# Optimization experiments

Measured on AMD Instinct MI355X. Metric: run time of the kernel, lower is better.

Reference implementation:

```python
import jax, jax.numpy as jnp
import numpy as np


def setup_inputs() -> dict:
    key = jax.random.key(0)
    ks = jax.random.split(key, 5)
    B, S, D = 4, 2048, 1024
    x = jax.random.normal(ks[0], (B, S, D), dtype=jnp.float32)
    wq = jax.random.normal(ks[1], (D, D), dtype=jnp.float32) * (D ** -0.5)
    wk = jax.random.normal(ks[2], (D, D), dtype=jnp.float32) * (D ** -0.5)
    wv = jax.random.normal(ks[3], (D, D), dtype=jnp.float32) * (D ** -0.5)
    wo = jax.random.normal(ks[4], (D, D), dtype=jnp.float32) * (D ** -0.5)
    return {"x": x, "wq": wq, "wk": wk, "wv": wv, "wo": wo, "n_heads": 16}


def reference(x, wq, wk, wv, wo, n_heads):
    B, S, D = x.shape
    hd = D // n_heads
    # projections (module computes x @ w.T)
    q = (x @ wq.T).reshape(B, S, n_heads, hd).transpose(0, 2, 1, 3)  # b h s d
    k = (x @ wk.T).reshape(B, S, n_heads, hd).transpose(0, 2, 1, 3)
    v = (x @ wv.T).reshape(B, S, n_heads, hd).transpose(0, 2, 1, 3)
    # NOTE: module scales by sqrt(d_model), not sqrt(head_dim)
    scores = jnp.einsum("bhqd,bhkd->bhqk", q, k) / jnp.sqrt(jnp.float32(D))
    # module bug preserved: masked_fill(mask == 0, -1e9) with mask = triu(diag=1)
    # fills positions where mask is False (lower triangle incl. diagonal).
    triu_mask = jnp.triu(jnp.ones((S, S), dtype=bool), k=1)  # True strictly above diag
    scores = jnp.where(triu_mask, scores, jnp.float32(-1e9))
    attn = jax.nn.softmax(scores, axis=-1)
    out = jnp.einsum("bhqk,bhkd->bhqd", attn, v)  # b h s d
    out = out.transpose(0, 2, 1, 3).reshape(B, S, D)
    return out @ wo.T
```

## Files before the change

kernel.cpp:

```cpp
#include <hip/hip_runtime.h>
#include <hip/hip_bf16.h>

typedef __attribute__((ext_vector_type(8))) short short8;
typedef __attribute__((ext_vector_type(4))) short bfx4;
typedef __attribute__((ext_vector_type(4))) float floatx4;
typedef __attribute__((ext_vector_type(4))) __fp16 h4_t;
typedef __attribute__((ext_vector_type(2))) __fp16 h2_t;
typedef __attribute__((ext_vector_type(8))) __fp16 h8_t;

#define BATCH 4
#define SEQ 2048
#define D_MODEL 1024
#define NH 16
#define HD 64
#define ELEMS 8388608
#define WELEMS 1048576

__device__ __forceinline__ unsigned short f2bf(float f) {
    union { float f; unsigned u; } x; x.f = f;
    unsigned r = x.u + 0x7FFFu + ((x.u >> 16) & 1u);
    return (unsigned short)(r >> 16);
}
__device__ __forceinline__ unsigned short f2h(float f) {
    union { __fp16 h; unsigned short u; } x;
    x.h = (__fp16)f;
    return x.u;
}

#if __has_builtin(__builtin_amdgcn_exp2f)
__device__ __forceinline__ float fexp2(float x) { return __builtin_amdgcn_exp2f(x); }
#else
__device__ __forceinline__ float fexp2(float x) { return exp2f(x); }
#endif

__device__ __forceinline__ void gll16(const void* g, const void* l) {
    __builtin_amdgcn_global_load_lds(
        (const __attribute__((address_space(1))) void*)g,
        (__attribute__((address_space(3))) void*)l,
        16, 0, 0);
}

__global__ __launch_bounds__(256)
void cvt_kernel(const float* __restrict__ x,  const float* __restrict__ wq,
                const float* __restrict__ wk, const float* __restrict__ wv,
                const float* __restrict__ wo,
                unsigned short* __restrict__ xbf,
                unsigned short* __restrict__ wqkv,
                unsigned short* __restrict__ wobf)
{
    size_t idx = ((size_t)blockIdx.x * 256 + threadIdx.x) * 8;
    const float* src; unsigned short* dst; size_t off;
    if (idx < (size_t)ELEMS)                    { src = x;  dst = xbf;             off = idx; }
    else if (idx < (size_t)ELEMS + WELEMS)      { src = wq; dst = wqkv;            off = idx - ELEMS; }
    else if (idx < (size_t)ELEMS + 2 * WELEMS)  { src = wk; dst = wqkv + WELEMS;   off = idx - ELEMS - WELEMS; }
    else if (idx < (size_t)ELEMS + 3 * WELEMS)  { src = wv; dst = wqkv + 2*WELEMS; off = idx - ELEMS - 2*WELEMS; }
    else                                        { src = wo; dst = wobf;            off = idx - ELEMS - 3*WELEMS; }
    floatx4 a = *(const floatx4*)(src + off);
    floatx4 b = *(const floatx4*)(src + off + 4);
    short8 v;
#pragma unroll
    for (int d = 0; d < 4; d++) { v[d] = (short)f2bf(a[d]); v[4+d] = (short)f2bf(b[d]); }
    *(short8*)(dst + off) = v;
}

__global__ __launch_bounds__(256, 2)
void gemm_qkv2_kernel(const unsigned short* __restrict__ A,
                      const unsigned short* __restrict__ B,
                      unsigned short* __restrict__ Qb,
                      unsigned short* __restrict__ Kb,
                      unsigned short* __restrict__ Vb)
{
    __shared__ __align__(16) unsigned short As[128 * 64];
    __shared__ __align__(16) unsigned short Bs[256 * 64];

    const int t = threadIdx.x;
    const int wave = t >> 6, lane = t & 63;
    const int lm = lane & 15, lq = lane >> 4;
    const int wrow = (wave >> 1) * 64, wcol = (wave & 1) * 128;
    const int m0 = blockIdx.x * 128, n0 = blockIdx.y * 256;
    const int lrow = lane >> 3, lg = lane & 7;
    const int gsw = lg ^ lrow;

    floatx4 acc[4][8] = {};

    for (int k0 = 0; k0 < 1024; k0 += 64) {
        __syncthreads();
#pragma unroll
        for (int i = 0; i < 4; i++) {
            int rows8 = wave * 32 + i * 8;
            gll16(A + (size_t)(m0 + rows8 + lrow) * 1024 + k0 + gsw * 8, As + rows8 * 64);
        }
#pragma unroll
        for (int i = 0; i < 8; i++) {
            int rows8 = wave * 64 + i * 8;
            gll16(B + (size_t)(n0 + rows8 + lrow) * 1024 + k0 + gsw * 8, Bs + rows8 * 64);
        }
        __syncthreads();

#pragma unroll
        for (int c = 0; c < 2; c++) {
            short8 af[4], bfr[8];
#pragma unroll
            for (int i = 0; i < 4; i++) {
                int ra = wrow + i * 16 + lm;
                int g = c * 4 + lq;
                af[i] = *(const short8*)(As + (ra * 8 + (g ^ (ra & 7))) * 8);
            }
#pragma unroll
            for (int j = 0; j < 8; j++) {
                int rb = wcol + j * 16 + lm;
                int g = c * 4 + lq;
                bfr[j] = *(const short8*)(Bs + (rb * 8 + (g ^ (rb & 7))) * 8);
            }
#pragma unroll
            for (int i = 0; i < 4; i++)
#pragma unroll
                for (int j = 0; j < 8; j++)
                    acc[i][j] = __builtin_amdgcn_mfma_f32_16x16x32_bf16(
                        af[i], bfr[j], acc[i][j], 0, 0, 0);
        }
    }

    const int z = n0 >> 10;
#pragma unroll
    for (int i = 0; i < 4; i++)
#pragma unroll
        for (int j = 0; j < 8; j++)
#pragma unroll
            for (int r = 0; r < 4; r++) {
                int gm = m0 + wrow + i * 16 + lq * 4 + r;
                int gn = n0 + wcol + j * 16 + lm;
                int nl = gn & 1023, h = nl >> 6, d = nl & 63;
                int b = gm >> 11, s = gm & 2047;
                float v = acc[i][j][r];
                size_t bh = (size_t)(b * NH + h);
                if (z == 0)      Qb[(bh * SEQ + s) * HD + d] = f2bf(v);
                else if (z == 1) Kb[(bh * SEQ + s) * HD + d] = f2bf(v);
                else             Vb[(bh * HD + d) * SEQ + s] = f2h(v);
            }
}

__global__ __launch_bounds__(256, 2)
void gemm_out2_kernel(const unsigned short* __restrict__ A,
                      const unsigned short* __restrict__ B,
                      float* __restrict__ Out)
{
    __shared__ __align__(16) unsigned short As[128 * 64];
    __shared__ __align__(16) unsigned short Bs[256 * 64];

    const int t = threadIdx.x;
    const int wave = t >> 6, lane = t & 63;
    const int lm = lane & 15, lq = lane >> 4;
    const int wrow = (wave >> 1) * 64, wcol = (wave & 1) * 128;
    const int m0 = blockIdx.x * 128, n0 = blockIdx.y * 256;
    const int lrow = lane >> 3, lg = lane & 7;
    const int gsw = lg ^ lrow;

    floatx4 acc[4][8] = {};

    for (int k0 = 0; k0 < 1024; k0 += 64) {
        __syncthreads();
#pragma unroll
        for (int i = 0; i < 4; i++) {
            int rows8 = wave * 32 + i * 8;
            gll16(A + (size_t)(m0 + rows8 + lrow) * 1024 + k0 + gsw * 8, As + rows8 * 64);
        }
#pragma unroll
        for (int i = 0; i < 8; i++) {
            int rows8 = wave * 64 + i * 8;
            gll16(B + (size_t)(n0 + rows8 + lrow) * 1024 + k0 + gsw * 8, Bs + rows8 * 64);
        }
        __syncthreads();

#pragma unroll
        for (int c = 0; c < 2; c++) {
            short8 af[4], bfr[8];
#pragma unroll
            for (int i = 0; i < 4; i++) {
                int ra = wrow + i * 16 + lm;
                int g = c * 4 + lq;
                af[i] = *(const short8*)(As + (ra * 8 + (g ^ (ra & 7))) * 8);
            }
#pragma unroll
            for (int j = 0; j < 8; j++) {
                int rb = wcol + j * 16 + lm;
                int g = c * 4 + lq;
                bfr[j] = *(const short8*)(Bs + (rb * 8 + (g ^ (rb & 7))) * 8);
            }
#pragma unroll
            for (int i = 0; i < 4; i++)
#pragma unroll
                for (int j = 0; j < 8; j++)
                    acc[i][j] = __builtin_amdgcn_mfma_f32_16x16x32_bf16(
                        af[i], bfr[j], acc[i][j], 0, 0, 0);
        }
    }

#pragma unroll
    for (int i = 0; i < 4; i++)
#pragma unroll
        for (int j = 0; j < 8; j++)
#pragma unroll
            for (int r = 0; r < 4; r++) {
                int gm = m0 + wrow + i * 16 + lq * 4 + r;
                int gn = n0 + wcol + j * 16 + lm;
                Out[(size_t)gm * D_MODEL + gn] = acc[i][j][r];
            }
}

#define PROCESS_Q(QI, BQ, ACC, LACC, DOMASK, KT)                               \
    do {                                                                       \
        _Pragma("unroll")                                                      \
        for (int jt = 0; jt < 8; jt++) {                                       \
            floatx4 sc = {};                                                   \
            _Pragma("unroll")                                                  \
            for (int c = 0; c < 2; c++) {                                      \
                int row_ = jt * 16 + lm;                                       \
                int g_ = c * 4 + lq;                                           \
                short8 kf = *(const short8*)(Ks + (row_ * 8 + (g_ ^ (row_ & 7))) * 8); \
                sc = __builtin_amdgcn_mfma_f32_16x16x32_bf16(kf, BQ[c], sc, 0, 0, 0); \
            }                                                                  \
            if (DOMASK) {                                                      \
                _Pragma("unroll")                                              \
                for (int r = 0; r < 4; r++) {                                  \
                    int kj = (KT) * 128 + jt * 16 + lq * 4 + r;                \
                    if (!(kj > (QI))) sc[r] = -3.2e10f;                        \
                }                                                              \
            }                                                                  \
            float p0 = fexp2(sc[0] * kA), p1 = fexp2(sc[1] * kA);              \
            float p2 = fexp2(sc[2] * kA), p3 = fexp2(sc[3] * kA);              \
            LACC += (p0 + p1) + (p2 + p3);                                     \
            h2_t a01 = __builtin_amdgcn_cvt_pkrtz(p0, p1);                     \
            h2_t a23 = __builtin_amdgcn_cvt_pkrtz(p2, p3);                     \
            h4_t pf;                                                           \
            pf[0] = a01[0]; pf[1] = a01[1]; pf[2] = a23[0]; pf[3] = a23[1];    \
            _Pragma("unroll")                                                  \
            for (int jd = 0; jd < 4; jd++) {                                   \
                int rowv_ = jd * 16 + lm;                                      \
                int g16_ = jt * 2 + (lq >> 1);                                 \
                int slot_ = rowv_ * 16 + (g16_ ^ lm);                          \
                h4_t vf = *(const h4_t*)((const __fp16*)Vs + slot_ * 8 + (lq & 1) * 4); \
                ACC[jd] = __builtin_amdgcn_mfma_f32_16x16x16f16(vf, pf, ACC[jd], 0, 0, 0); \
            }                                                                  \
        }                                                                      \
    } while (0)

__global__ __launch_bounds__(256, 2)
void attn5_kernel(const unsigned short* __restrict__ Q,
                  const unsigned short* __restrict__ K,
                  const unsigned short* __restrict__ V,
                  unsigned short* __restrict__ O)
{
    __shared__ __align__(16) unsigned short Ks[128 * 64];
    __shared__ __align__(16) unsigned short Vs[64 * 128];

    const int t = threadIdx.x;
    const int wave = t >> 6, lane = t & 63;
    const int lm = lane & 15, lq = lane >> 4;
    const int bh = blockIdx.y;
    const int jlo = blockIdx.x, jhi = 31 - jlo;
    const int qlo = jlo * 64 + wave * 16 + lm;
    const int qhi = jhi * 64 + wave * 16 + lm;

    const unsigned short* Qh = Q + (size_t)bh * SEQ * HD;
    const unsigned short* Kh = K + (size_t)bh * SEQ * HD;
    const unsigned short* Vh = V + (size_t)bh * HD * SEQ;

    short8 bq_lo[2], bq_hi[2];
    bq_lo[0] = *(const short8*)(Qh + (size_t)qlo * HD + lq * 8);
    bq_lo[1] = *(const short8*)(Qh + (size_t)qlo * HD + 32 + lq * 8);
    bq_hi[0] = *(const short8*)(Qh + (size_t)qhi * HD + lq * 8);
    bq_hi[1] = *(const short8*)(Qh + (size_t)qhi * HD + 32 + lq * 8);

    floatx4 acc_lo[4] = {}, acc_hi[4] = {};
    float l_lo = 0.f, l_hi = 0.f;
    const float kA = 0.04508422002778011f;

    const int lrow = lane >> 3, lg = lane & 7;
    const int kt_min = jlo >> 1;
    const int kthi_min = 15 - kt_min;

    for (int kt = 15; kt >= kt_min; kt--) {
        __syncthreads();
#pragma unroll
        for (int i = 0; i < 4; i++) {
            int rows8 = wave * 32 + i * 8;
            gll16(Kh + (size_t)(kt * 128 + rows8 + lrow) * HD + (lg ^ lrow) * 8,
                  Ks + rows8 * 64);
        }
#pragma unroll
        for (int i = 0; i < 4; i++) {
            int rows4 = wave * 16 + i * 4;
            int row = rows4 + (lane >> 4);
            int g = (lane & 15) ^ (row & 15);
            gll16(Vh + (size_t)row * SEQ + kt * 128 + g * 8, Vs + rows4 * 128);
        }
        __syncthreads();

        PROCESS_Q(qlo, bq_lo, acc_lo, l_lo, (kt == kt_min), kt);
        if (kt >= kthi_min)
            PROCESS_Q(qhi, bq_hi, acc_hi, l_hi, (kt == kthi_min), kt);
    }

    const int b = bh >> 4, h = bh & 15;
    {
        float l = l_lo;
        l += __shfl_xor(l, 16); l += __shfl_xor(l, 32);
        float inv = 1.0f / l;
#pragma unroll
        for (int jd = 0; jd < 4; jd++) {
            bfx4 o;
#pragma unroll
            for (int r = 0; r < 4; r++) o[r] = (short)f2bf(acc_lo[jd][r] * inv);
            *(bfx4*)(O + (size_t)(b * SEQ + qlo) * D_MODEL + h * HD + jd * 16 + lq * 4) = o;
        }
    }
    {
        float l = l_hi;
        l += __shfl_xor(l, 16); l += __shfl_xor(l, 32);
        float inv = 1.0f / l;
#pragma unroll
        for (int jd = 0; jd < 4; jd++) {
            bfx4 o;
#pragma unroll
            for (int r = 0; r < 4; r++) o[r] = (short)f2bf(acc_hi[jd][r] * inv);
            *(bfx4*)(O + (size_t)(b * SEQ + qhi) * D_MODEL + h * HD + jd * 16 + lq * 4) = o;
        }
    }
}

__global__ __launch_bounds__(256, 2)
void row2047_kernel(const unsigned short* __restrict__ V,
                    unsigned short* __restrict__ O)
{
    __shared__ float red[256];
    const int bh = blockIdx.x;
    const int b = bh >> 4, h = bh & 15;
    const int t = threadIdx.x;
    const int d = t & 63, seg = t >> 6;
    const __fp16* Vh = (const __fp16*)V + (size_t)bh * HD * SEQ + (size_t)d * SEQ + seg * 512;
    float s = 0.f;
    for (int i = 0; i < 512; i += 8) {
        h8_t v = *(const h8_t*)(Vh + i);
#pragma unroll
        for (int j = 0; j < 8; j++) s += (float)v[j];
    }
    red[t] = s;
    __syncthreads();
    if (seg == 0) {
        float tot = red[d] + red[64 + d] + red[128 + d] + red[192 + d];
        O[(size_t)(b * SEQ + 2047) * D_MODEL + h * HD + d] = f2bf(tot * (1.f / 2048.f));
    }
}

__global__ __launch_bounds__(256, 2)
void gemm_qkv_kernel(const float* __restrict__ A,
                     const float* __restrict__ W0,
                     const float* __restrict__ W1,
                     const float* __restrict__ W2,
                     unsigned short* __restrict__ O0,
                     unsigned short* __restrict__ O1,
                     unsigned short* __restrict__ O2)
{
    const int K = 1024;
    const float* W;
    unsigned short* Out;
    if (blockIdx.z == 0)      { W = W0; Out = O0; }
    else if (blockIdx.z == 1) { W = W1; Out = O1; }
    else                      { W = W2; Out = O2; }

    __shared__ __align__(16) unsigned short As[128 * 64];
    __shared__ __align__(16) unsigned short Bs[128 * 64];

    const int t = threadIdx.x;
    const int wave = t >> 6, lane = t & 63;
    const int lm = lane & 15, lq = lane >> 4;
    const int wrow = (wave >> 1) * 64, wcol = (wave & 1) * 64;
    const int m0 = blockIdx.x * 128, n0 = blockIdx.y * 128;

    floatx4 acc[4][4] = {};

    for (int k0 = 0; k0 < K; k0 += 64) {
        __syncthreads();
#pragma unroll
        for (int rr = 0; rr < 4; rr++) {
            int p = rr * 256 + t;
            int row = p >> 3, g = p & 7;
            const float* pa = A + (size_t)(m0 + row) * K + k0 + g * 8;
            const float* pw = W + (size_t)(n0 + row) * K + k0 + g * 8;
            floatx4 a0 = *(const floatx4*)pa, a1 = *(const floatx4*)(pa + 4);
            floatx4 w0 = *(const floatx4*)pw, w1 = *(const floatx4*)(pw + 4);
            short8 va, vb;
#pragma unroll
            for (int d = 0; d < 4; d++) {
                va[d]     = (short)f2bf(a0[d]);
                va[4 + d] = (short)f2bf(a1[d]);
                vb[d]     = (short)f2bf(w0[d]);
                vb[4 + d] = (short)f2bf(w1[d]);
            }
            int dst = row * 8 + (g ^ (row & 7));
            *(short8*)(As + dst * 8) = va;
            *(short8*)(Bs + dst * 8) = vb;
        }
        __syncthreads();

        short8 af[4][2], bf[4][2];
#pragma unroll
        for (int i = 0; i < 4; i++)
#pragma unroll
            for (int c = 0; c < 2; c++) {
                int ra = wrow + i * 16 + lm;
                int rb = wcol + i * 16 + lm;
                int g = c * 4 + lq;
                af[i][c] = *(const short8*)(As + (ra * 8 + (g ^ (ra & 7))) * 8);
                bf[i][c] = *(const short8*)(Bs + (rb * 8 + (g ^ (rb & 7))) * 8);
            }
#pragma unroll
        for (int i = 0; i < 4; i++)
#pragma unroll
            for (int j = 0; j < 4; j++)
#pragma unroll
                for (int c = 0; c < 2; c++)
                    acc[i][j] = __builtin_amdgcn_mfma_f32_16x16x32_bf16(
                        af[i][c], bf[j][c], acc[i][j], 0, 0, 0);
    }

    const int zi = blockIdx.z;
#pragma unroll
    for (int i = 0; i < 4; i++)
#pragma unroll
        for (int j = 0; j < 4; j++)
#pragma unroll
            for (int r = 0; r < 4; r++) {
                int gm = m0 + wrow + i * 16 + lq * 4 + r;
                int gn = n0 + wcol + j * 16 + lm;
                int b = gm >> 11, s = gm & 2047;
                int h = gn >> 6, d = gn & 63;
                if (zi == 2) {
                    Out[((size_t)(b * NH + h) * HD + d) * SEQ + s] = f2h(acc[i][j][r]);
                } else {
                    Out[((size_t)(b * NH + h) * SEQ + s) * HD + d] = f2bf(acc[i][j][r]);
                }
            }
}

__global__ __launch_bounds__(256, 2)
void gemm_out_kernel(const unsigned short* __restrict__ Abf,
                     const float* __restrict__ W,
                     float* __restrict__ Out)
{
    const int K = 1024;
    __shared__ __align__(16) unsigned short As[128 * 64];
    __shared__ __align__(16) unsigned short Bs[128 * 64];

    const int t = threadIdx.x;
    const int wave = t >> 6, lane = t & 63;
    const int lm = lane & 15, lq = lane >> 4;
    const int wrow = (wave >> 1) * 64, wcol = (wave & 1) * 64;
    const int m0 = blockIdx.x * 128, n0 = blockIdx.y * 128;

    floatx4 acc[4][4] = {};

    for (int k0 = 0; k0 < K; k0 += 64) {
        __syncthreads();
#pragma unroll
        for (int rr = 0; rr < 4; rr++) {
            int p = rr * 256 + t;
            int row = p >> 3, g = p & 7;
            short8 va = *(const short8*)(Abf + (size_t)(m0 + row) * K + k0 + g * 8);
            const float* pw = W + (size_t)(n0 + row) * K + k0 + g * 8;
            floatx4 w0 = *(const floatx4*)pw, w1 = *(const floatx4*)(pw + 4);
            short8 vb;
#pragma unroll
            for (int d = 0; d < 4; d++) {
                vb[d]     = (short)f2bf(w0[d]);
                vb[4 + d] = (short)f2bf(w1[d]);
            }
            int dst = row * 8 + (g ^ (row & 7));
            *(short8*)(As + dst * 8) = va;
            *(short8*)(Bs + dst * 8) = vb;
        }
        __syncthreads();

        short8 af[4][2], bf[4][2];
#pragma unroll
        for (int i = 0; i < 4; i++)
#pragma unroll
            for (int c = 0; c < 2; c++) {
                int ra = wrow + i * 16 + lm;
                int rb = wcol + i * 16 + lm;
                int g = c * 4 + lq;
                af[i][c] = *(const short8*)(As + (ra * 8 + (g ^ (ra & 7))) * 8);
                bf[i][c] = *(const short8*)(Bs + (rb * 8 + (g ^ (rb & 7))) * 8);
            }
#pragma unroll
        for (int i = 0; i < 4; i++)
#pragma unroll
            for (int j = 0; j < 4; j++)
#pragma unroll
                for (int c = 0; c < 2; c++)
                    acc[i][j] = __builtin_amdgcn_mfma_f32_16x16x32_bf16(
                        af[i][c], bf[j][c], acc[i][j], 0, 0, 0);
    }

#pragma unroll
    for (int i = 0; i < 4; i++)
#pragma unroll
        for (int j = 0; j < 4; j++)
#pragma unroll
            for (int r = 0; r < 4; r++) {
                int gm = m0 + wrow + i * 16 + lq * 4 + r;
                int gn = n0 + wcol + j * 16 + lm;
                Out[(size_t)gm * D_MODEL + gn] = acc[i][j][r];
            }
}

extern "C" void kernel_launch(void* const* d_in, const int* in_sizes, int n_in,
                              void* d_out, int out_size, void* d_ws, size_t ws_size,
                              hipStream_t stream) {
    const float* x  = (const float*)d_in[0];
    const float* wq = (const float*)d_in[1];
    const float* wk = (const float*)d_in[2];
    const float* wv = (const float*)d_in[3];
    const float* wo = (const float*)d_in[4];

    unsigned short* ws = (unsigned short*)d_ws;
    const bool fast = ws_size >= (size_t)36 * 1024 * 1024 * 2;

    if (fast) {
        unsigned short* xbf  = ws;
        unsigned short* wqkv = ws + (size_t)ELEMS;
        unsigned short* wobf = ws + (size_t)ELEMS + 3 * WELEMS;
        unsigned short* Qb   = ws + (size_t)ELEMS + 4 * WELEMS;
        unsigned short* Kb   = Qb + ELEMS;
        unsigned short* Vb   = Kb + ELEMS;
        unsigned short* Ob   = xbf;

        cvt_kernel<<<6144, 256, 0, stream>>>(x, wq, wk, wv, wo, xbf, wqkv, wobf);
        gemm_qkv2_kernel<<<dim3(64, 12), 256, 0, stream>>>(xbf, wqkv, Qb, Kb, Vb);
        attn5_kernel<<<dim3(16, BATCH * NH), 256, 0, stream>>>(Qb, Kb, Vb, Ob);
        row2047_kernel<<<BATCH * NH, 256, 0, stream>>>(Vb, Ob);
        gemm_out2_kernel<<<dim3(64, 4), 256, 0, stream>>>(Ob, wobf, (float*)d_out);
    } else {
        unsigned short* Qb = ws;
        unsigned short* Kb = Qb + ELEMS;
        unsigned short* Vb = Kb + ELEMS;
        unsigned short* Ob = Vb + ELEMS;

        gemm_qkv_kernel<<<dim3(64, 8, 3), 256, 0, stream>>>(x, wq, wk, wv, Qb, Kb, Vb);
        attn5_kernel<<<dim3(16, BATCH * NH), 256, 0, stream>>>(Qb, Kb, Vb, Ob);
        row2047_kernel<<<BATCH * NH, 256, 0, stream>>>(Vb, Ob);
        gemm_out_kernel<<<dim3(64, 8), 256, 0, stream>>>(Ob, wo, (float*)d_out);
    }
}
```

Baseline: 316.9 us.

## Replace GEMM kernels with 256x256-tile, 8-wave, double-buffered pipelined GEMM

Replaces the two single-buffered 128x256 bf16 GEMMs (QKV projection and output projection) with one templated 512-thread kernel. It uses 256x256 tiles, double-buffered LDS and interleaved quarter-tile MFMA blocks. Global-to-LDS loads for the next k-tiles are issued between compute phases, with explicit vmcnt waits, barriers and setprio, so memory traffic overlaps the MFMAs. LDS use rises to 128KB per block and the grids shrink (384 and 128 blocks), which risks occupancy and tail effects on the smaller output GEMM.

```diff
diff --git a/kernel.cpp b/kernel.cpp
--- a/kernel.cpp
+++ b/kernel.cpp
@@ -39,6 +39,10 @@
         (__attribute__((address_space(3))) void*)l,
         16, 0, 0);
 }
+
+#define BAR() __builtin_amdgcn_s_barrier()
+#define WAIT_LGKM0() asm volatile("s_waitcnt lgkmcnt(0)" ::: "memory")
+#define WAIT_VM(N) asm volatile("s_waitcnt vmcnt(" #N ")" ::: "memory")
 
 __global__ __launch_bounds__(256)
 void cvt_kernel(const float* __restrict__ x,  const float* __restrict__ wq,
@@ -63,149 +67,146 @@
     *(short8*)(dst + off) = v;
 }
 
-__global__ __launch_bounds__(256, 2)
-void gemm_qkv2_kernel(const unsigned short* __restrict__ A,
-                      const unsigned short* __restrict__ B,
-                      unsigned short* __restrict__ Qb,
-                      unsigned short* __restrict__ Kb,
-                      unsigned short* __restrict__ Vb)
+#define READ_A(MH, BUF)                                                          \
+    do {                                                                         \
+        _Pragma("unroll")                                                        \
+        for (int mi_ = 0; mi_ < 4; mi_++) {                                      \
+            _Pragma("unroll")                                                    \
+            for (int c_ = 0; c_ < 2; c_++) {                                     \
+                int ra_ = wm * 128 + ((MH) * 4 + mi_) * 16 + lm;                 \
+                int g_ = c_ * 4 + lq;                                            \
+                a[mi_][c_] = *(const short8*)(&As[BUF][(ra_ * 8 + (g_ ^ (ra_ & 7))) * 8]); \
+            }                                                                    \
+        }                                                                        \
+    } while (0)
+
+#define READ_B(NHF, BUF)                                                         \
+    do {                                                                         \
+        _Pragma("unroll")                                                        \
+        for (int nj_ = 0; nj_ < 2; nj_++) {                                      \
+            _Pragma("unroll")                                                    \
+            for (int c_ = 0; c_ < 2; c_++) {                                     \
+                int rb_ = wn * 64 + ((NHF) * 2 + nj_) * 16 + lm;                 \
+                int g_ = c_ * 4 + lq;                                            \
+                b[(NHF) * 2 + nj_][c_] = *(const short8*)(&Bs[BUF][(rb_ * 8 + (g_ ^ (rb_ & 7))) * 8]); \
+            }                                                                    \
+        }                                                                        \
+    } while (0)
+
+#define QUAD(MH, NHF)                                                            \
+    do {                                                                         \
+        __builtin_amdgcn_s_setprio(1);                                           \
+        _Pragma("unroll")                                                        \
+        for (int mi_ = 0; mi_ < 4; mi_++) {                                      \
+            _Pragma("unroll")                                                    \
+            for (int nj_ = 0; nj_ < 2; nj_++) {                                  \
+                _Pragma("unroll")                                                \
+                for (int c_ = 0; c_ < 2; c_++)                                   \
+                    acc[(MH) * 4 + mi_][(NHF) * 2 + nj_] =                       \
+                        __builtin_amdgcn_mfma_f32_16x16x32_bf16(                 \
+                            a[mi_][c_], b[(NHF) * 2 + nj_][c_],                  \
+                            acc[(MH) * 4 + mi_][(NHF) * 2 + nj_], 0, 0, 0);      \
+            }                                                                    \
+        }                                                                        \
+        __builtin_amdgcn_s_setprio(0);                                           \
+    } while (0)
+
+#define STAGE(DSTBASE, SRC, GROW0, KT)                                           \
+    do {                                                                         \
+        _Pragma("unroll")                                                        \
+        for (int i_ = 0; i_ < 2; i_++) {                                         \
+            int r8_ = wave * 16 + i_ * 8;                                        \
+            gll16((SRC) + (size_t)((GROW0) + r8_ + lrow) * 1024 + (KT) * 64 + ((lg ^ lrow) << 3), \
+                  (DSTBASE) + r8_ * 64);                                         \
+        }                                                                        \
+    } while (0)
+
+template <int MODE>
+__global__ __launch_bounds__(512, 2)
+void gemm8_kernel(const unsigned short* __restrict__ A,
+                  const unsigned short* __restrict__ Bw,
+                  unsigned short* __restrict__ Qb,
+                  unsigned short* __restrict__ Kb,
+                  unsigned short* __restrict__ Vb,
+                  float* __restrict__ Out)
 {
-    __shared__ __align__(16) unsigned short As[128 * 64];
-    __shared__ __align__(16) unsigned short Bs[256 * 64];
+    __shared__ __align__(16) unsigned short As[2][256 * 64];
+    __shared__ __align__(16) unsigned short Bs[2][256 * 64];
 
     const int t = threadIdx.x;
     const int wave = t >> 6, lane = t & 63;
     const int lm = lane & 15, lq = lane >> 4;
-    const int wrow = (wave >> 1) * 64, wcol = (wave & 1) * 128;
-    const int m0 = blockIdx.x * 128, n0 = blockIdx.y * 256;
+    const int wm = wave >> 2, wn = wave & 3;
     const int lrow = lane >> 3, lg = lane & 7;
-    const int gsw = lg ^ lrow;
-
-    floatx4 acc[4][8] = {};
-
-    for (int k0 = 0; k0 < 1024; k0 += 64) {
-        __syncthreads();
-#pragma unroll
-        for (int i = 0; i < 4; i++) {
-            int rows8 = wave * 32 + i * 8;
-            gll16(A + (size_t)(m0 + rows8 + lrow) * 1024 + k0 + gsw * 8, As + rows8 * 64);
-        }
-#pragma unroll
-        for (int i = 0; i < 8; i++) {
-            int rows8 = wave * 64 + i * 8;
-            gll16(B + (size_t)(n0 + rows8 + lrow) * 1024 + k0 + gsw * 8, Bs + rows8 * 64);
-        }
-        __syncthreads();
-
-#pragma unroll
-        for (int c = 0; c < 2; c++) {
-            short8 af[4], bfr[8];
-#pragma unroll
-            for (int i = 0; i < 4; i++) {
-                int ra = wrow + i * 16 + lm;
-                int g = c * 4 + lq;
-                af[i] = *(const short8*)(As + (ra * 8 + (g ^ (ra & 7))) * 8);
-            }
-#pragma unroll
-            for (int j = 0; j < 8; j++) {
-                int rb = wcol + j * 16 + lm;
-                int g = c * 4 + lq;
-                bfr[j] = *(const short8*)(Bs + (rb * 8 + (g ^ (rb & 7))) * 8);
-            }
-#pragma unroll
-            for (int i = 0; i < 4; i++)
-#pragma unroll
-                for (int j = 0; j < 8; j++)
-                    acc[i][j] = __builtin_amdgcn_mfma_f32_16x16x32_bf16(
-                        af[i], bfr[j], acc[i][j], 0, 0, 0);
-        }
-    }
-
-    const int z = n0 >> 10;
-#pragma unroll
-    for (int i = 0; i < 4; i++)
-#pragma unroll
-        for (int j = 0; j < 8; j++)
-#pragma unroll
-            for (int r = 0; r < 4; r++) {
-                int gm = m0 + wrow + i * 16 + lq * 4 + r;
-                int gn = n0 + wcol + j * 16 + lm;
-                int nl = gn & 1023, h = nl >> 6, d = nl & 63;
-                int b = gm >> 11, s = gm & 2047;
-                float v = acc[i][j][r];
-                size_t bh = (size_t)(b * NH + h);
-                if (z == 0)      Qb[(bh * SEQ + s) * HD + d] = f2bf(v);
-                else if (z == 1) Kb[(bh * SEQ + s) * HD + d] = f2bf(v);
-                else             Vb[(bh * HD + d) * SEQ + s] = f2h(v);
-            }
-}
-
-__global__ __launch_bounds__(256, 2)
-void gemm_out2_kernel(const unsigned short* __restrict__ A,
-                      const unsigned short* __restrict__ B,
-                      float* __restrict__ Out)
-{
-    __shared__ __align__(16) unsigned short As[128 * 64];
-    __shared__ __align__(16) unsigned short Bs[256 * 64];
-
-    const int t = threadIdx.x;
-    const int wave = t >> 6, lane = t & 63;
-    const int lm = lane & 15, lq = lane >> 4;
-    const int wrow = (wave >> 1) * 64, wcol = (wave & 1) * 128;
-    const int m0 = blockIdx.x * 128, n0 = blockIdx.y * 256;
-    const int lrow = lane >> 3, lg = lane & 7;
-    const int gsw = lg ^ lrow;
-
-    floatx4 acc[4][8] = {};
-
-    for (int k0 = 0; k0 < 1024; k0 += 64) {
-        __syncthreads();
-#pragma unroll
-        for (int i = 0; i < 4; i++) {
-            int rows8 = wave * 32 + i * 8;
-            gll16(A + (size_t)(m0 + rows8 + lrow) * 1024 + k0 + gsw * 8, As + rows8 * 64);
-        }
-#pragma unroll
-        for (int i = 0; i < 8; i++) {
-            int rows8 = wave * 64 + i * 8;
-            gll16(B + (size_t)(n0 + rows8 + lrow) * 1024 + k0 + gsw * 8, Bs + rows8 * 64);
-        }
-        __syncthreads();
-
-#pragma unroll
-        for (int c = 0; c < 2; c++) {
-            short8 af[4], bfr[8];
-#pragma unroll
-            for (int i = 0; i < 4; i++) {
-                int ra = wrow + i * 16 + lm;
-                int g = c * 4 + lq;
-                af[i] = *(const short8*)(As + (ra * 8 + (g ^ (ra & 7))) * 8);
-            }
-#pragma unroll
-            for (int j = 0; j < 8; j++) {
-                int rb = wcol + j * 16 + lm;
-                int g = c * 4 + lq;
-                bfr[j] = *(const short8*)(Bs + (rb * 8 + (g ^ (rb & 7))) * 8);
-            }
-#pragma unroll
-            for (int i = 0; i < 4; i++)
-#pragma unroll
-                for (int j = 0; j < 8; j++)
-                    acc[i][j] = __builtin_amdgcn_mfma_f32_16x16x32_bf16(
-                        af[i], bfr[j], acc[i][j], 0, 0, 0);
-        }
-    }
-
-#pragma unroll
-    for (int i = 0; i < 4; i++)
-#pragma unroll
-        for (int j = 0; j < 8; j++)
-#pragma unroll
-            for (int r = 0; r < 4; r++) {
-                int gm = m0 + wrow + i * 16 + lq * 4 + r;
-                int gn = n0 + wcol + j * 16 + lm;
-                Out[(size_t)gm * D_MODEL + gn] = acc[i][j][r];
-            }
+    const int m0 = blockIdx.x * 256, n0 = blockIdx.y * 256;
+
+    floatx4 acc[8][4] = {};
+    short8 a[4][2], b[4][2];
+
+    STAGE(&Bs[0][0],        Bw, n0,       0);
+    STAGE(&Bs[0][128 * 64], Bw, n0 + 128, 0);
+    STAGE(&As[0][0],        A,  m0,       0);
+    STAGE(&As[0][128 * 64], A,  m0 + 128, 0);
+    STAGE(&Bs[1][0],        Bw, n0,       1);
+    STAGE(&Bs[1][128 * 64], Bw, n0 + 128, 1);
+    WAIT_VM(4);
+    BAR();
+
+#pragma unroll 2
+    for (int kt = 0; kt < 16; kt++) {
+        const int cur = kt & 1, nxt = cur ^ 1;
+        READ_A(0, cur); READ_B(0, cur);
+        if (kt + 1 < 16) STAGE(&As[nxt][0], A, m0, kt + 1);
+        BAR(); WAIT_LGKM0();
+        QUAD(0, 0);
+        BAR();
+        READ_B(1, cur);
+        if (kt + 1 < 16) STAGE(&As[nxt][128 * 64], A, m0 + 128, kt + 1);
+        BAR(); WAIT_LGKM0();
+        QUAD(0, 1);
+        BAR();
+        READ_A(1, cur);
+        if (kt + 2 < 16) STAGE(&Bs[cur][0], Bw, n0, kt + 2);
+        BAR(); WAIT_LGKM0();
+        QUAD(1, 0);
+        BAR();
+        if (kt + 2 < 16) STAGE(&Bs[cur][128 * 64], Bw, n0 + 128, kt + 2);
+        BAR();
+        QUAD(1, 1);
+        if (kt + 2 < 16) { WAIT_VM(4); } else { WAIT_VM(0); }
+        BAR();
+    }
+
+    if (MODE == 0) {
+        const int z = n0 >> 10;
+#pragma unroll
+        for (int mi = 0; mi < 8; mi++)
+#pragma unroll
+            for (int nj = 0; nj < 4; nj++)
+#pragma unroll
+                for (int r = 0; r < 4; r++) {
+                    int gm = m0 + wm * 128 + mi * 16 + lq * 4 + r;
+                    int gn = n0 + wn * 64 + nj * 16 + lm;
+                    int nl = gn & 1023, h = nl >> 6, d = nl & 63;
+                    int bb = gm >> 11, s = gm & 2047;
+                    float v = acc[mi][nj][r];
+                    size_t bh = (size_t)(bb * NH + h);
+                    if (z == 0)      Qb[(bh * SEQ + s) * HD + d] = f2bf(v);
+                    else if (z == 1) Kb[(bh * SEQ + s) * HD + d] = f2bf(v);
+                    else             Vb[(bh * HD + d) * SEQ + s] = f2h(v);
+                }
+    } else {
+#pragma unroll
+        for (int mi = 0; mi < 8; mi++)
+#pragma unroll
+            for (int nj = 0; nj < 4; nj++)
+#pragma unroll
+                for (int r = 0; r < 4; r++) {
+                    int gm = m0 + wm * 128 + mi * 16 + lq * 4 + r;
+                    int gn = n0 + wn * 64 + nj * 16 + lm;
+                    Out[(size_t)gm * D_MODEL + gn] = acc[mi][nj][r];
+                }
+    }
 }
 
 #define PROCESS_Q(QI, BQ, ACC, LACC, DOMASK, KT)                               \
@@ -537,10 +538,10 @@
         unsigned short* Ob   = xbf;
 
         cvt_kernel<<<6144, 256, 0, stream>>>(x, wq, wk, wv, wo, xbf, wqkv, wobf);
-        gemm_qkv2_kernel<<<dim3(64, 12), 256, 0, stream>>>(xbf, wqkv, Qb, Kb, Vb);
+        gemm8_kernel<0><<<dim3(32, 12), 512, 0, stream>>>(xbf, wqkv, Qb, Kb, Vb, nullptr);
         attn5_kernel<<<dim3(16, BATCH * NH), 256, 0, stream>>>(Qb, Kb, Vb, Ob);
         row2047_kernel<<<BATCH * NH, 256, 0, stream>>>(Vb, Ob);
-        gemm_out2_kernel<<<dim3(64, 4), 256, 0, stream>>>(Ob, wobf, (float*)d_out);
+        gemm8_kernel<1><<<dim3(32, 4), 512, 0, stream>>>(Ob, wobf, nullptr, nullptr, nullptr, (float*)d_out);
     } else {
         unsigned short* Qb = ws;
         unsigned short* Kb = Qb + ELEMS;
```

New measurement: 341.5 us. 7.8% more time.

## Double-buffer K/V tiles in attention kernel to overlap loads with compute

Applied to the files above, without the earlier changes.

Splits the shared-memory K and V tiles into two buffers. The next key tile is issued with async global-to-LDS loads before the current tile is processed, and one barrier per iteration replaces the two barriers that used to bracket the loads. The goal is to hide global load latency behind the MFMA and exp work of each tile. In exchange, LDS use per block doubles, which may limit how many blocks fit on each CU.

```diff
diff --git a/kernel.cpp b/kernel.cpp
--- a/kernel.cpp
+++ b/kernel.cpp
@@ -39,6 +39,7 @@
         (__attribute__((address_space(3))) void*)l,
         16, 0, 0);
 }
+
 
 __global__ __launch_bounds__(256)
 void cvt_kernel(const float* __restrict__ x,  const float* __restrict__ wq,
@@ -217,7 +218,7 @@
             for (int c = 0; c < 2; c++) {                                      \
                 int row_ = jt * 16 + lm;                                       \
                 int g_ = c * 4 + lq;                                           \
-                short8 kf = *(const short8*)(Ks + (row_ * 8 + (g_ ^ (row_ & 7))) * 8); \
+                short8 kf = *(const short8*)(Ksb + (row_ * 8 + (g_ ^ (row_ & 7))) * 8); \
                 sc = __builtin_amdgcn_mfma_f32_16x16x32_bf16(kf, BQ[c], sc, 0, 0, 0); \
             }                                                                  \
             if (DOMASK) {                                                      \
@@ -239,20 +240,38 @@
                 int rowv_ = jd * 16 + lm;                                      \
                 int g16_ = jt * 2 + (lq >> 1);                                 \
                 int slot_ = rowv_ * 16 + (g16_ ^ lm);                          \
-                h4_t vf = *(const h4_t*)((const __fp16*)Vs + slot_ * 8 + (lq & 1) * 4); \
+                h4_t vf = *(const h4_t*)(Vsb + slot_ * 8 + (lq & 1) * 4);      \
                 ACC[jd] = __builtin_amdgcn_mfma_f32_16x16x16f16(vf, pf, ACC[jd], 0, 0, 0); \
             }                                                                  \
         }                                                                      \
     } while (0)
 
+#define STAGE_KV(BUF, KT)                                                      \
+    do {                                                                       \
+        _Pragma("unroll")                                                      \
+        for (int i_ = 0; i_ < 4; i_++) {                                       \
+            int rows8_ = wave * 32 + i_ * 8;                                   \
+            gll16(Kh + (size_t)((KT) * 128 + rows8_ + lrow) * HD + (lg ^ lrow) * 8, \
+                  &Ks[BUF][rows8_ * 64]);                                      \
+        }                                                                      \
+        _Pragma("unroll")                                                      \
+        for (int i_ = 0; i_ < 4; i_++) {                                       \
+            int rows4_ = wave * 16 + i_ * 4;                                   \
+            int row_ = rows4_ + (lane >> 4);                                   \
+            int g_ = (lane & 15) ^ (row_ & 15);                                \
+            gll16(Vh + (size_t)row_ * SEQ + (KT) * 128 + g_ * 8,               \
+                  &Vs[BUF][rows4_ * 128]);                                     \
+        }                                                                      \
+    } while (0)
+
 __global__ __launch_bounds__(256, 2)
-void attn5_kernel(const unsigned short* __restrict__ Q,
+void attn6_kernel(const unsigned short* __restrict__ Q,
                   const unsigned short* __restrict__ K,
                   const unsigned short* __restrict__ V,
                   unsigned short* __restrict__ O)
 {
-    __shared__ __align__(16) unsigned short Ks[128 * 64];
-    __shared__ __align__(16) unsigned short Vs[64 * 128];
+    __shared__ __align__(16) unsigned short Ks[2][128 * 64];
+    __shared__ __align__(16) unsigned short Vs[2][64 * 128];
 
     const int t = threadIdx.x;
     const int wave = t >> 6, lane = t & 63;
@@ -280,26 +299,21 @@
     const int kt_min = jlo >> 1;
     const int kthi_min = 15 - kt_min;
 
+    STAGE_KV(0, 15);
+    __syncthreads();
+
     for (int kt = 15; kt >= kt_min; kt--) {
-        __syncthreads();
-#pragma unroll
-        for (int i = 0; i < 4; i++) {
-            int rows8 = wave * 32 + i * 8;
-            gll16(Kh + (size_t)(kt * 128 + rows8 + lrow) * HD + (lg ^ lrow) * 8,
-                  Ks + rows8 * 64);
-        }
-#pragma unroll
-        for (int i = 0; i < 4; i++) {
-            int rows4 = wave * 16 + i * 4;
-            int row = rows4 + (lane >> 4);
-            int g = (lane & 15) ^ (row & 15);
-            gll16(Vh + (size_t)row * SEQ + kt * 128 + g * 8, Vs + rows4 * 128);
-        }
-        __syncthreads();
+        const int cb = (15 - kt) & 1;
+        if (kt - 1 >= kt_min) STAGE_KV(cb ^ 1, kt - 1);
+
+        const unsigned short* Ksb = &Ks[cb][0];
+        const __fp16* Vsb = (const __fp16*)&Vs[cb][0];
 
         PROCESS_Q(qlo, bq_lo, acc_lo, l_lo, (kt == kt_min), kt);
         if (kt >= kthi_min)
             PROCESS_Q(qhi, bq_hi, acc_hi, l_hi, (kt == kthi_min), kt);
+
+        __syncthreads();
     }
 
     const int b = bh >> 4, h = bh & 15;
@@ -538,7 +552,7 @@
 
         cvt_kernel<<<6144, 256, 0, stream>>>(x, wq, wk, wv, wo, xbf, wqkv, wobf);
         gemm_qkv2_kernel<<<dim3(64, 12), 256, 0, stream>>>(xbf, wqkv, Qb, Kb, Vb);
-        attn5_kernel<<<dim3(16, BATCH * NH), 256, 0, stream>>>(Qb, Kb, Vb, Ob);
+        attn6_kernel<<<dim3(16, BATCH * NH), 256, 0, stream>>>(Qb, Kb, Vb, Ob);
         row2047_kernel<<<BATCH * NH, 256, 0, stream>>>(Vb, Ob);
         gemm_out2_kernel<<<dim3(64, 4), 256, 0, stream>>>(Ob, wobf, (float*)d_out);
     } else {
@@ -548,7 +562,7 @@
         unsigned short* Ob = Vb + ELEMS;
 
         gemm_qkv_kernel<<<dim3(64, 8, 3), 256, 0, stream>>>(x, wq, wk, wv, Qb, Kb, Vb);
-        attn5_kernel<<<dim3(16, BATCH * NH), 256, 0, stream>>>(Qb, Kb, Vb, Ob);
+        attn6_kernel<<<dim3(16, BATCH * NH), 256, 0, stream>>>(Qb, Kb, Vb, Ob);
         row2047_kernel<<<BATCH * NH, 256, 0, stream>>>(Vb, Ob);
         gemm_out_kernel<<<dim3(64, 8), 256, 0, stream>>>(Ob, wo, (float*)d_out);
     }
```

Result: slower. 336.9 us (+6.3%).
